# Kernel tuning notes

Hardware: AMD Instinct MI355X
Metric: run time of the kernel (lower is better)

The kernel has to match this reference:

```python
import jax, jax.numpy as jnp
import numpy as np

N_, C_, H_, W_ = 8, 256, 64, 64
HEADS = 8
KS = 3
K2 = KS * KS
OUT = 256
HD = OUT // HEADS
STRIDE = 1
PAD = 1


def setup_inputs() -> dict:
    key = jax.random.key(0)
    ks = jax.random.split(key, 8)
    s = 0.05
    return {
        "input_features": jax.random.normal(ks[0], (N_, C_, H_, W_), jnp.float32),
        "Wq": jax.random.normal(ks[1], (OUT, C_), jnp.float32) * s,
        "Wk": jax.random.normal(ks[2], (OUT, C_), jnp.float32) * s,
        "Wv": jax.random.normal(ks[3], (OUT, C_), jnp.float32) * s,
        "off_w": jax.random.normal(ks[4], (HEADS * K2 * 2, C_, KS, KS), jnp.float32) * 0.01,
        "off_b": jnp.zeros((HEADS * K2 * 2,), jnp.float32),
        "attn_w": jax.random.normal(ks[5], (HEADS * K2, C_, KS, KS), jnp.float32) * 0.01,
        "attn_b": jnp.zeros((HEADS * K2,), jnp.float32),
        "Wo": jax.random.normal(ks[6], (OUT, OUT), jnp.float32) * s,
    }


def _conv2d(x, w, b):
    out = jax.lax.conv_general_dilated(
        x, w, (STRIDE, STRIDE), [(PAD, PAD), (PAD, PAD)],
        dimension_numbers=("NCHW", "OIHW", "NCHW"))
    return out + b[None, :, None, None]


def reference(input_features, Wq, Wk, Wv, off_w, off_b, attn_w, attn_b, Wo):
    x = input_features
    N, C, H, W = x.shape
    # query/key are projected but never used downstream in the original module
    q = jnp.einsum("oc,nchw->nohw", Wq, x)
    k = jnp.einsum("oc,nchw->nohw", Wk, x)
    v = jnp.einsum("oc,nchw->nohw", Wv, x)  # [N, OUT, H, W]

    offsets = _conv2d(x, off_w, off_b)                       # [N, HEADS*K2*2, Ho, Wo]
    aw = jax.nn.sigmoid(_conv2d(x, attn_w, attn_b))          # [N, HEADS*K2, Ho, Wo]
    Ho, Wo_sp = offsets.shape[2], offsets.shape[3]

    gx_base = jnp.linspace(-1.0, 1.0, Wo_sp)
    gy_base = jnp.linspace(-1.0, 1.0, Ho)

    # per-head, per-point (x,y) offsets, scaled by 2/[W,H] as in the source
    off = offsets.reshape(N, HEADS, K2, 2, Ho, Wo_sp)
    gx = gx_base[None, None, None, None, :] + off[:, :, :, 0] * (2.0 / W)  # [N,H,K2,Ho,Wo]
    gy = gy_base[None, None, None, :, None] + off[:, :, :, 1] * (2.0 / H)

    # grid_sample bilinear, align_corners=True, padding_mode='zeros'
    xp = (gx + 1.0) * 0.5 * (W - 1)
    yp = (gy + 1.0) * 0.5 * (H - 1)
    x0 = jnp.floor(xp).astype(jnp.int32)
    y0 = jnp.floor(yp).astype(jnp.int32)
    x1 = x0 + 1
    y1 = y0 + 1
    wx1 = xp - x0
    wx0 = 1.0 - wx1
    wy1 = yp - y0
    wy0 = 1.0 - wy1

    vf = v.reshape(N, HEADS, HD, H * W)

    def corner(yi, xi, wgt):
        valid = ((yi >= 0) & (yi < H) & (xi >= 0) & (xi < W)).astype(v.dtype)
        idx = (jnp.clip(yi, 0, H - 1) * W + jnp.clip(xi, 0, W - 1)).reshape(N, HEADS, -1)
        g = jnp.take_along_axis(vf, idx[:, :, None, :], axis=3)
        g = g.reshape(N, HEADS, HD, K2, Ho, Wo_sp)
        return g * (wgt * valid)[:, :, None]

    sampled = (corner(y0, x0, wy0 * wx0) + corner(y0, x1, wy0 * wx1)
               + corner(y1, x0, wy1 * wx0) + corner(y1, x1, wy1 * wx1))

    awr = aw.reshape(N, HEADS, K2, Ho, Wo_sp)
    head_out = jnp.einsum("nhckxy,nhkxy->nhcxy", sampled, awr)  # weighted sum over K2 points
    combined = head_out.reshape(N, OUT, Ho, Wo_sp)
    return jnp.einsum("oc,nchw->nohw", Wo, combined)
```

## Files before the change

### kernel.cpp

```cpp
#include <hip/hip_runtime.h>
#include <math.h>

#define N_    8
#define C_    256
#define H_    64
#define W_    64
#define HW    4096
#define OUT_  256
#define HEADS 8
#define HD    32
#define K2    9
#define OFFCH 144
#define AWCH  72
#define KTOT  2304
#define WPROWS 256
#define ABASE 16896

typedef __bf16 bf16x8 __attribute__((ext_vector_type(8)));
typedef __bf16 bf16x4 __attribute__((ext_vector_type(4)));
typedef float  f32x4  __attribute__((ext_vector_type(4)));

__device__ __forceinline__ void gload_lds16(const void* g, void* l) {
  __builtin_amdgcn_global_load_lds(
      (const __attribute__((address_space(1))) void*)g,
      (__attribute__((address_space(3))) void*)l, 16, 0, 0);
}

__device__ __forceinline__ void conv_body(
    __bf16* smem, const __bf16* __restrict__ xp, const __bf16* __restrict__ Wp,
    const float* __restrict__ biasp, const __bf16* __restrict__ zbuf,
    __bf16* __restrict__ P2, int yt, int bn, int n, int tid)
{
  const int y0 = yt << 1;
  const int lw = tid & 63, wv = tid >> 6;
  const int lr = lw & 15, lg = lw >> 4;

  f32x4 acc[8][2];
#pragma unroll
  for (int m = 0; m < 8; ++m)
#pragma unroll
    for (int nt = 0; nt < 2; ++nt) acc[m][nt] = (f32x4){0.f, 0.f, 0.f, 0.f};

  if (tid < 64) {
    int p = tid & 3, cs = (tid >> 2) & 1, r = (tid >> 3) & 3, buf = tid >> 5;
    int col = cs ? 65 : 0;
    *(uint4*)&smem[((buf * 4 + r) * 66 + col) * 32 + p * 8] =
        make_uint4(0u, 0u, 0u, 0u);
  }

  int aoff[3][4];
#pragma unroll
  for (int d = 0; d < 3; ++d)
#pragma unroll
    for (int mm = 0; mm < 4; ++mm) {
      int col = (mm << 4) + lr + d;
      int p = lg ^ ((col >> 1) & 3);
      aoff[d][mm] = col * 32 + p * 8;
    }
  int boff[2];
#pragma unroll
  for (int nt = 0; nt < 2; ++nt) {
    int col = (nt << 4) + lr;
    int p = lg ^ ((col >> 1) & 3);
    boff[nt] = ABASE + wv * 3072 + col * 32 + p * 8;
  }

  const int scg = lw & 3;
  const __bf16* gB[2];
#pragma unroll
  for (int jj = 0; jj < 2; ++jj) {
    int col = (jj << 4) + (lw >> 2);
    int cg = scg ^ ((col >> 1) & 3);
    gB[jj] = Wp + (size_t)(bn * 128 + wv * 32 + col) * KTOT + (cg << 3);
  }
  const __bf16* gA[4];
  int aAdd;
  {
    int y = y0 - 1 + wv;
    bool valid = ((unsigned)y < (unsigned)H_);
    aAdd = valid ? 1 : 0;
#pragma unroll
    for (int k = 0; k < 4; ++k) {
      int col = 1 + (k << 4) + (lw >> 2);
      int cg = scg ^ ((col >> 1) & 3);
      gA[k] = valid
          ? xp + ((size_t)(n * HW) + y * W_ + (col - 1)) * C_ + (cg << 3)
          : zbuf;
    }
  }

  auto stageB = [&](int elemOff, int pbuf) {
#pragma unroll
    for (int jj = 0; jj < 2; ++jj)
      gload_lds16(gB[jj] + elemOff,
                  &smem[ABASE + wv * 3072 + pbuf * 1024 + (jj << 9)]);
  };
  auto stageA = [&](int c0elem, int buf) {
    const int add = aAdd ? c0elem : 0;
#pragma unroll
    for (int k = 0; k < 4; ++k)
      gload_lds16(gA[k] + add,
                  &smem[((buf * 4 + wv) * 66 + 1 + (k << 4)) * 32]);
  };

  stageA(0, 0);
  stageB(0 * C_ + 0, 0);
  stageB(1 * C_ + 0, 1);
  asm volatile("s_waitcnt vmcnt(4)" ::: "memory");
  __builtin_amdgcn_s_barrier();
  asm volatile("" ::: "memory");

  for (int cc = 0; cc < 4; ++cc) {
    const bool lastcc = (cc == 3);
#pragma unroll
    for (int sub = 0; sub < 2; ++sub) {
      const int ci = (cc << 1) + sub;
      const int abuf = sub;
#pragma unroll
      for (int tt = 0; tt < 9; ++tt) {
        const int dy = tt / 3, dxp = tt - dy * 3;
        const int pbR = tt % 3;
        const int pbW = (tt + 2) % 3;
        const bool lastSlice = lastcc && (sub == 1);

        if (tt == 1 && ci < 7) stageA((ci + 1) << 5, sub ^ 1);

        if (!(lastSlice && tt >= 7)) {
          const int tn  = (tt < 7) ? (tt + 2) : (tt - 7);
          const int cin = (tt < 7) ? ci : (ci + 1);
          stageB(tn * C_ + (cin << 5), pbW);
        }

        if (lastSlice && tt == 8)
          asm volatile("s_waitcnt vmcnt(0)" ::: "memory");
        else if (lastSlice && tt == 7)
          asm volatile("s_waitcnt vmcnt(2)" ::: "memory");
        else if ((tt == 1 || tt == 2) && ci < 7)
          asm volatile("s_waitcnt vmcnt(8)" ::: "memory");
        else
          asm volatile("s_waitcnt vmcnt(4)" ::: "memory");

        bf16x8 a[8], b[2];
#pragma unroll
        for (int m = 0; m < 8; ++m) {
          const int rr = (m >> 2) + dy;
          a[m] = *(const bf16x8*)&smem[aoff[dxp][m & 3] +
                                       (abuf * 4 + rr) * 2112];
        }
#pragma unroll
        for (int nt = 0; nt < 2; ++nt)
          b[nt] = *(const bf16x8*)&smem[boff[nt] + (pbR << 10)];

        __builtin_amdgcn_s_setprio(1);
#pragma unroll
        for (int m = 0; m < 8; ++m)
#pragma unroll
          for (int nt = 0; nt < 2; ++nt)
            acc[m][nt] = __builtin_amdgcn_mfma_f32_16x16x32_bf16(
                a[m], b[nt], acc[m][nt], 0, 0, 0);
        __builtin_amdgcn_s_setprio(0);

        if (tt == 8 && !lastSlice) {
          __builtin_amdgcn_s_barrier();
          asm volatile("" ::: "memory");
        }
      }
    }
  }

#pragma unroll
  for (int nt = 0; nt < 2; ++nt) {
    const int co = bn * 128 + wv * 32 + (nt << 4) + lr;
    if (co < 216) {
      const float bias = biasp[co];
      int idx;
      if (co < OFFCH) {
        int hh = co / 18;
        idx = (hh << 5) + (co - 18 * hh);
      } else {
        int r = co - OFFCH;
        int hh = r / 9;
        idx = (hh << 5) + 18 + (r - 9 * hh);
      }
#pragma unroll
      for (int m = 0; m < 8; ++m) {
#pragma unroll
        for (int reg = 0; reg < 4; ++reg) {
          const int sl = (m << 4) + (lg << 2) + reg;
          const int yout = y0 + (sl >> 6), xo = sl & 63;
          float v = acc[m][nt][reg] + bias;
          if (co >= OFFCH) v = 1.f / (1.f + expf(-v));
          P2[((size_t)n * HW + yout * W_ + xo) * 256 + idx] = (__bf16)v;
        }
      }
    }
  }
}

template <int MODE>
__device__ __forceinline__ void gemm_body(
    __bf16* smem, const __bf16* __restrict__ A, const __bf16* __restrict__ Wb,
    __bf16* __restrict__ out_b, float* __restrict__ out_f,
    int st, int bn, int n, int tid)
{
  const int s0 = st << 7;
  const int lw = tid & 63, wv = tid >> 6;
  const int lr = lw & 15, lg = lw >> 4;
  const int sm_base = wv << 5;

  f32x4 acc[2][8];
#pragma unroll
  for (int m = 0; m < 2; ++m)
#pragma unroll
    for (int nt = 0; nt < 8; ++nt) acc[m][nt] = (f32x4){0.f, 0.f, 0.f, 0.f};

  int aoff[2];
#pragma unroll
  for (int m = 0; m < 2; ++m) {
    int row = sm_base + (m << 4) + lr;
    int p = lg ^ ((row >> 1) & 3);
    aoff[m] = row * 32 + p * 8;
  }
  int boff[8];
#pragma unroll
  for (int nt = 0; nt < 8; ++nt) {
    int row = (nt << 4) + lr;
    int p = lg ^ ((row >> 1) & 3);
    boff[nt] = 12288 + row * 32 + p * 8;
  }

  const __bf16* gA[2];
  const __bf16* gB[2];
#pragma unroll
  for (int jj = 0; jj < 2; ++jj) {
    int j = wv * 2 + jj;
    int row = (j << 4) + (lw >> 2);
    int cg = (lw & 3) ^ ((row >> 1) & 3);
    gA[jj] = A + ((size_t)n * HW + s0 + row) * 256 + (cg << 3);
    gB[jj] = Wb + ((size_t)((bn << 7) + row)) * 256 + (cg << 3);
  }

  auto stage = [&](int k, int buf) {
    const int koff = k << 5;
#pragma unroll
    for (int jj = 0; jj < 2; ++jj)
      gload_lds16(gA[jj] + koff, &smem[buf * 4096 + ((wv * 2 + jj) << 9)]);
#pragma unroll
    for (int jj = 0; jj < 2; ++jj)
      gload_lds16(gB[jj] + koff,
                  &smem[12288 + buf * 4096 + ((wv * 2 + jj) << 9)]);
  };

  stage(0, 0);
  stage(1, 1);

#pragma unroll
  for (int k = 0; k < 8; ++k) {
    if (k < 7)
      asm volatile("s_waitcnt vmcnt(4)" ::: "memory");
    else
      asm volatile("s_waitcnt vmcnt(0)" ::: "memory");
    __builtin_amdgcn_s_barrier();
    asm volatile("" ::: "memory");

    if (k + 2 < 8) stage(k + 2, (k + 2) % 3);

    const int buf = k % 3;
    bf16x8 a[2], b[8];
#pragma unroll
    for (int m = 0; m < 2; ++m)
      a[m] = *(const bf16x8*)&smem[aoff[m] + buf * 4096];
#pragma unroll
    for (int nt = 0; nt < 8; ++nt)
      b[nt] = *(const bf16x8*)&smem[boff[nt] + buf * 4096];

    __builtin_amdgcn_s_setprio(1);
#pragma unroll
    for (int m = 0; m < 2; ++m)
#pragma unroll
      for (int nt = 0; nt < 8; ++nt)
        acc[m][nt] = __builtin_amdgcn_mfma_f32_16x16x32_bf16(
            a[m], b[nt], acc[m][nt], 0, 0, 0);
    __builtin_amdgcn_s_setprio(0);
  }

#pragma unroll
  for (int m = 0; m < 2; ++m) {
#pragma unroll
    for (int nt = 0; nt < 8; ++nt) {
      const int co = (bn << 7) + (nt << 4) + lr;
      if (MODE == 0) {
#pragma unroll
        for (int reg = 0; reg < 4; ++reg) {
          const int sm = sm_base + (m << 4) + (lg << 2) + reg;
          out_b[((size_t)n * HW + s0 + sm) * 256 + co] = (__bf16)acc[m][nt][reg];
        }
      } else {
        const int sm = sm_base + (m << 4) + (lg << 2);
        float4 v4 = make_float4(acc[m][nt][0], acc[m][nt][1],
                                acc[m][nt][2], acc[m][nt][3]);
        *(float4*)&out_f[((size_t)(n * 256 + co)) * HW + s0 + sm] = v4;
      }
    }
  }
}

__global__ __launch_bounds__(256) void fused_pre_kernel(
    const float* __restrict__ x, __bf16* __restrict__ xp,
    const float* __restrict__ off_w, const float* __restrict__ off_b,
    const float* __restrict__ attn_w, const float* __restrict__ attn_b,
    const float* __restrict__ Wv, const float* __restrict__ Wo,
    __bf16* __restrict__ Wp, float* __restrict__ biasp,
    __bf16* __restrict__ zbuf, __bf16* __restrict__ Wvb,
    __bf16* __restrict__ Wob)
{
  const int b = blockIdx.x;
  const int tid = threadIdx.x;
  __shared__ float tile[64][65];

  if (b < 2048) {
    const int c0 = (b & 3) << 6;
    const int y  = (b >> 2) & 63;
    const int n  = b >> 8;
    const int tx = tid & 63, tg = tid >> 6;
#pragma unroll
    for (int i = 0; i < 16; ++i) {
      int cl = tg + (i << 2);
      tile[cl][tx] = x[((size_t)(n * C_ + c0 + cl) * H_ + y) * W_ + tx];
    }
    __syncthreads();
#pragma unroll
    for (int i = 0; i < 16; ++i) {
      int xl = tg + (i << 2);
      xp[((size_t)(n * HW) + y * W_ + xl) * C_ + c0 + tx] = (__bf16)tile[tx][xl];
    }
  } else {
    const int bb = b - 2048;
    const int c = tid;
    if (bb < 256) {
      const int co = bb;
      if (co == 0) {
        *(uint4*)&zbuf[(size_t)c * 8] = make_uint4(0u, 0u, 0u, 0u);
      }
      const float* base = nullptr;
      if (co < OFFCH)      base = off_w  + ((size_t)co * C_ + c) * 9;
      else if (co < 216)   base = attn_w + ((size_t)(co - OFFCH) * C_ + c) * 9;
#pragma unroll
      for (int t = 0; t < 9; ++t) {
        float w = base ? base[t] : 0.f;
        Wp[(size_t)co * KTOT + t * C_ + c] = (__bf16)w;
      }
      if (c == 0) {
        float bv = 0.f;
        if (co < OFFCH) bv = off_b[co];
        else if (co < 216) bv = attn_b[co - OFFCH];
        biasp[co] = bv;
      }
    } else if (bb < 512) {
      const int i = (bb - 256) * 256 + c;
      Wvb[i] = (__bf16)Wv[i];
    } else {
      const int i = (bb - 512) * 256 + c;
      Wob[i] = (__bf16)Wo[i];
    }
  }
}

__global__ __launch_bounds__(256) void fused_cv_kernel(
    const __bf16* __restrict__ xp, const __bf16* __restrict__ Wp,
    const float* __restrict__ biasp, const __bf16* __restrict__ zbuf,
    __bf16* __restrict__ P2, const __bf16* __restrict__ Wvb,
    __bf16* __restrict__ vtb)
{
  __shared__ __align__(16) __bf16 smem[16896 + 12288];
  const int bn = blockIdx.y;
  if (bn < 2)
    conv_body(smem, xp, Wp, biasp, zbuf, P2, blockIdx.x, bn, blockIdx.z,
              threadIdx.x);
  else
    gemm_body<0>(smem, xp, Wvb, vtb, nullptr, blockIdx.x, bn - 2, blockIdx.z,
                 threadIdx.x);
}

__global__ __launch_bounds__(256) void wo_kernel(
    const __bf16* __restrict__ comb, const __bf16* __restrict__ Wob,
    float* __restrict__ out)
{
  __shared__ __align__(16) __bf16 smem[24576];
  gemm_body<1>(smem, comb, Wob, nullptr, out, blockIdx.x, blockIdx.y,
               blockIdx.z, threadIdx.x);
}

__global__ __launch_bounds__(256) void sample_kernel(
    const __bf16* __restrict__ vtb, const __bf16* __restrict__ P2,
    __bf16* __restrict__ comb)
{
  const int b = blockIdx.x;
  const int y = b & 63;
  const int h = (b >> 6) & 7;
  const int n = b >> 9;
  const int tid = threadIdx.x;
  const int xq = tid >> 2, cg = tid & 3;
  const int lw = tid & 63, wv = tid >> 6;

  __shared__ __align__(16) __bf16 vsl[8 * 64 * 32];

  const int xs = (wv << 4) + (lw >> 2);
  const int cs = lw & 3;
  const __bf16* vrow0 =
      vtb + ((size_t)n * HW) * 256 + (h << 5) + (cs << 3) + (size_t)xs * 256;
#pragma unroll
  for (int r = 0; r < 8; ++r) {
    int yy = y - 3 + r;
    if ((unsigned)yy < (unsigned)H_)
      gload_lds16(vrow0 + (size_t)yy * (64 * 256),
                  &vsl[(r * 64 + (wv << 4)) * 32]);
  }

  const __bf16* prow = P2 + ((size_t)n * HW + y * 64 + xq) * 256 + (h << 5);
  bf16x8 p0 = *(const bf16x8*)(prow);
  bf16x8 p1 = *(const bf16x8*)(prow + 8);
  bf16x8 p2 = *(const bf16x8*)(prow + 16);
  bf16x4 p3 = *(const bf16x4*)(prow + 24);

  __syncthreads();

  float acc[8];
#pragma unroll
  for (int j = 0; j < 8; ++j) acc[j] = 0.f;

  const __bf16* vbase = vtb + ((size_t)n * HW) * 256 + (h << 5) + (cg << 3);

#pragma unroll
  for (int k = 0; k < K2; ++k) {
    float offx, offy, a;
    if (k < 4)      { offx = (float)p0[2 * k];       offy = (float)p0[2 * k + 1]; }
    else if (k < 8) { offx = (float)p1[2 * (k - 4)]; offy = (float)p1[2 * (k - 4) + 1]; }
    else            { offx = (float)p2[0];           offy = (float)p2[1]; }
    if (k < 6)      a = (float)p2[2 + k];
    else            a = (float)p3[k - 6];

    const float xpf = (float)xq + offx * (63.f / 64.f);
    const float ypf = (float)y  + offy * (63.f / 64.f);
    const float fx0 = floorf(xpf), fy0 = floorf(ypf);
    const int x0 = (int)fx0, y0 = (int)fy0;
    const float wx1 = xpf - fx0, wx0 = 1.f - wx1;
    const float wy1 = ypf - fy0, wy0 = 1.f - wy1;

#pragma unroll
    for (int cy = 0; cy < 2; ++cy) {
      const int yi = y0 + cy;
      if ((unsigned)yi >= (unsigned)H_) continue;
      const float wy = cy ? wy1 : wy0;
      const int ridx = yi - (y - 3);
#pragma unroll
      for (int cx = 0; cx < 2; ++cx) {
        const int xi = x0 + cx;
        if ((unsigned)xi >= (unsigned)W_) continue;
        const float cw = a * wy * (cx ? wx1 : wx0);
        bf16x8 v;
        if ((unsigned)ridx < 8u) {
          v = *(const bf16x8*)&vsl[(ridx * 64 + xi) * 32 + (cg << 3)];
        } else {
          v = *(const bf16x8*)(vbase + (size_t)(yi * W_ + xi) * 256);
        }
#pragma unroll
        for (int j = 0; j < 8; ++j) acc[j] = fmaf(cw, (float)v[j], acc[j]);
      }
    }
  }

  bf16x8 r;
#pragma unroll
  for (int j = 0; j < 8; ++j) r[j] = (__bf16)acc[j];
  *(bf16x8*)&comb[((size_t)n * HW + y * 64 + xq) * 256 + (h << 5) + (cg << 3)] = r;
}

extern "C" void kernel_launch(void* const* d_in, const int* in_sizes, int n_in,
                              void* d_out, int out_size, void* d_ws,
                              size_t ws_size, hipStream_t stream)
{
  const float* x      = (const float*)d_in[0];
  const float* Wv     = (const float*)d_in[3];
  const float* off_w  = (const float*)d_in[4];
  const float* off_b  = (const float*)d_in[5];
  const float* attn_w = (const float*)d_in[6];
  const float* attn_b = (const float*)d_in[7];
  const float* Wo     = (const float*)d_in[8];
  float* out = (float*)d_out;

  __bf16* vtb   = (__bf16*)d_ws;
  __bf16* xp    = vtb + (size_t)N_ * HW * OUT_;
  __bf16* comb  = xp + (size_t)N_ * HW * C_;
  __bf16* P2    = comb + (size_t)N_ * HW * OUT_;
  __bf16* Wp    = P2 + (size_t)N_ * HW * 256;
  __bf16* Wvb   = Wp + (size_t)WPROWS * KTOT;
  __bf16* Wob   = Wvb + (size_t)OUT_ * C_;
  __bf16* zbuf  = Wob + (size_t)OUT_ * OUT_;
  float*  biasp = (float*)(zbuf + 2048);

  fused_pre_kernel<<<dim3(2816), 256, 0, stream>>>(
      x, xp, off_w, off_b, attn_w, attn_b, Wv, Wo, Wp, biasp, zbuf, Wvb, Wob);
  fused_cv_kernel<<<dim3(32, 4, N_), 256, 0, stream>>>(xp, Wp, biasp, zbuf, P2,
                                                       Wvb, vtb);
  sample_kernel<<<dim3(N_ * HEADS * H_), 256, 0, stream>>>(vtb, P2, comb);
  wo_kernel<<<dim3(32, 2, N_), 256, 0, stream>>>(comb, Wob, out);
}
```

Measured before the change: 112.9 us.

## Shrink conv tile to one output row per block to double conv block count

The implicit-GEMM conv blocks now compute a single output row (64 pixels) instead of two, so the conv part of the fused grid doubles from 2 to 4 y-slices. The A halo buffer drops from 4 rows to 3 rows, and each wave stages 3 row segments instead of 4, which shrinks shared memory and should raise occupancy and parallelism. In exchange, halo reuse per block falls (3 input rows per output row instead of 4 per 2), and each block re-streams the full weight tile for half the output.

```diff
diff --git a/kernel.cpp b/kernel.cpp
--- a/kernel.cpp
+++ b/kernel.cpp
@@ -14,7 +14,7 @@
 #define AWCH  72
 #define KTOT  2304
 #define WPROWS 256
-#define ABASE 16896
+#define ABASE2 12672
 
 typedef __bf16 bf16x8 __attribute__((ext_vector_type(8)));
 typedef __bf16 bf16x4 __attribute__((ext_vector_type(4)));
@@ -29,22 +29,21 @@
 __device__ __forceinline__ void conv_body(
     __bf16* smem, const __bf16* __restrict__ xp, const __bf16* __restrict__ Wp,
     const float* __restrict__ biasp, const __bf16* __restrict__ zbuf,
-    __bf16* __restrict__ P2, int yt, int bn, int n, int tid)
-{
-  const int y0 = yt << 1;
+    __bf16* __restrict__ P2, int yq, int bn, int n, int tid)
+{
   const int lw = tid & 63, wv = tid >> 6;
   const int lr = lw & 15, lg = lw >> 4;
 
-  f32x4 acc[8][2];
-#pragma unroll
-  for (int m = 0; m < 8; ++m)
+  f32x4 acc[4][2];
+#pragma unroll
+  for (int m = 0; m < 4; ++m)
 #pragma unroll
     for (int nt = 0; nt < 2; ++nt) acc[m][nt] = (f32x4){0.f, 0.f, 0.f, 0.f};
 
-  if (tid < 64) {
-    int p = tid & 3, cs = (tid >> 2) & 1, r = (tid >> 3) & 3, buf = tid >> 5;
+  if (tid < 48) {
+    int p = tid & 3, cs = (tid >> 2) & 1, r = (tid >> 3) % 3, buf = tid / 24;
     int col = cs ? 65 : 0;
-    *(uint4*)&smem[((buf * 4 + r) * 66 + col) * 32 + p * 8] =
+    *(uint4*)&smem[((buf * 3 + r) * 66 + col) * 32 + p * 8] =
         make_uint4(0u, 0u, 0u, 0u);
   }
 
@@ -62,7 +61,7 @@
   for (int nt = 0; nt < 2; ++nt) {
     int col = (nt << 4) + lr;
     int p = lg ^ ((col >> 1) & 3);
-    boff[nt] = ABASE + wv * 3072 + col * 32 + p * 8;
+    boff[nt] = ABASE2 + wv * 3072 + col * 32 + p * 8;
   }
 
   const int scg = lw & 3;
@@ -73,34 +72,35 @@
     int cg = scg ^ ((col >> 1) & 3);
     gB[jj] = Wp + (size_t)(bn * 128 + wv * 32 + col) * KTOT + (cg << 3);
   }
-  const __bf16* gA[4];
-  int aAdd;
-  {
-    int y = y0 - 1 + wv;
+  const __bf16* gA[3];
+  int aAdd[3];
+  int aDst[3];
+#pragma unroll
+  for (int k = 0; k < 3; ++k) {
+    int u = wv * 3 + k;
+    int r = u >> 2, j = u & 3;
+    int y = yq - 1 + r;
     bool valid = ((unsigned)y < (unsigned)H_);
-    aAdd = valid ? 1 : 0;
-#pragma unroll
-    for (int k = 0; k < 4; ++k) {
-      int col = 1 + (k << 4) + (lw >> 2);
-      int cg = scg ^ ((col >> 1) & 3);
-      gA[k] = valid
-          ? xp + ((size_t)(n * HW) + y * W_ + (col - 1)) * C_ + (cg << 3)
-          : zbuf;
-    }
+    aAdd[k] = valid ? 1 : 0;
+    int col = 1 + (j << 4) + (lw >> 2);
+    int cg = scg ^ ((col >> 1) & 3);
+    gA[k] = valid
+        ? xp + ((size_t)(n * HW) + y * W_ + (col - 1)) * C_ + (cg << 3)
+        : zbuf;
+    aDst[k] = (r * 66 + 1 + (j << 4)) * 32;
   }
 
   auto stageB = [&](int elemOff, int pbuf) {
 #pragma unroll
     for (int jj = 0; jj < 2; ++jj)
       gload_lds16(gB[jj] + elemOff,
-                  &smem[ABASE + wv * 3072 + pbuf * 1024 + (jj << 9)]);
+                  &smem[ABASE2 + wv * 3072 + pbuf * 1024 + (jj << 9)]);
   };
   auto stageA = [&](int c0elem, int buf) {
-    const int add = aAdd ? c0elem : 0;
-#pragma unroll
-    for (int k = 0; k < 4; ++k)
-      gload_lds16(gA[k] + add,
-                  &smem[((buf * 4 + wv) * 66 + 1 + (k << 4)) * 32]);
+#pragma unroll
+    for (int k = 0; k < 3; ++k)
+      gload_lds16(gA[k] + (aAdd[k] ? c0elem : 0),
+                  &smem[buf * (3 * 66 * 32) + aDst[k]]);
   };
 
   stageA(0, 0);
@@ -136,24 +136,22 @@
         else if (lastSlice && tt == 7)
           asm volatile("s_waitcnt vmcnt(2)" ::: "memory");
         else if ((tt == 1 || tt == 2) && ci < 7)
-          asm volatile("s_waitcnt vmcnt(8)" ::: "memory");
+          asm volatile("s_waitcnt vmcnt(7)" ::: "memory");
         else
           asm volatile("s_waitcnt vmcnt(4)" ::: "memory");
 
-        bf16x8 a[8], b[2];
-#pragma unroll
-        for (int m = 0; m < 8; ++m) {
-          const int rr = (m >> 2) + dy;
-          a[m] = *(const bf16x8*)&smem[aoff[dxp][m & 3] +
-                                       (abuf * 4 + rr) * 2112];
-        }
+        bf16x8 a[4], b[2];
+#pragma unroll
+        for (int m = 0; m < 4; ++m)
+          a[m] = *(const bf16x8*)&smem[aoff[dxp][m] +
+                                       (abuf * 3 + dy) * 2112];
 #pragma unroll
         for (int nt = 0; nt < 2; ++nt)
           b[nt] = *(const bf16x8*)&smem[boff[nt] + (pbR << 10)];
 
         __builtin_amdgcn_s_setprio(1);
 #pragma unroll
-        for (int m = 0; m < 8; ++m)
+        for (int m = 0; m < 4; ++m)
 #pragma unroll
           for (int nt = 0; nt < 2; ++nt)
             acc[m][nt] = __builtin_amdgcn_mfma_f32_16x16x32_bf16(
@@ -183,14 +181,13 @@
         idx = (hh << 5) + 18 + (r - 9 * hh);
       }
 #pragma unroll
-      for (int m = 0; m < 8; ++m) {
+      for (int m = 0; m < 4; ++m) {
 #pragma unroll
         for (int reg = 0; reg < 4; ++reg) {
-          const int sl = (m << 4) + (lg << 2) + reg;
-          const int yout = y0 + (sl >> 6), xo = sl & 63;
+          const int xo = (m << 4) + (lg << 2) + reg;
           float v = acc[m][nt][reg] + bias;
           if (co >= OFFCH) v = 1.f / (1.f + expf(-v));
-          P2[((size_t)n * HW + yout * W_ + xo) * 256 + idx] = (__bf16)v;
+          P2[((size_t)n * HW + yq * W_ + xo) * 256 + idx] = (__bf16)v;
         }
       }
     }
@@ -372,14 +369,16 @@
     __bf16* __restrict__ P2, const __bf16* __restrict__ Wvb,
     __bf16* __restrict__ vtb)
 {
-  __shared__ __align__(16) __bf16 smem[16896 + 12288];
+  __shared__ __align__(16) __bf16 smem[24960];
   const int bn = blockIdx.y;
-  if (bn < 2)
-    conv_body(smem, xp, Wp, biasp, zbuf, P2, blockIdx.x, bn, blockIdx.z,
-              threadIdx.x);
-  else
-    gemm_body<0>(smem, xp, Wvb, vtb, nullptr, blockIdx.x, bn - 2, blockIdx.z,
+  if (bn < 4) {
+    const int yq  = (blockIdx.x << 1) | (bn & 1);
+    const int cbn = bn >> 1;
+    conv_body(smem, xp, Wp, biasp, zbuf, P2, yq, cbn, blockIdx.z, threadIdx.x);
+  } else {
+    gemm_body<0>(smem, xp, Wvb, vtb, nullptr, blockIdx.x, bn - 4, blockIdx.z,
                  threadIdx.x);
+  }
 }
 
 __global__ __launch_bounds__(256) void wo_kernel(
@@ -501,7 +500,7 @@
 
   fused_pre_kernel<<<dim3(2816), 256, 0, stream>>>(
       x, xp, off_w, off_b, attn_w, attn_b, Wv, Wo, Wp, biasp, zbuf, Wvb, Wob);
-  fused_cv_kernel<<<dim3(32, 4, N_), 256, 0, stream>>>(xp, Wp, biasp, zbuf, P2,
+  fused_cv_kernel<<<dim3(32, 6, N_), 256, 0, stream>>>(xp, Wp, biasp, zbuf, P2,
                                                        Wvb, vtb);
   sample_kernel<<<dim3(N_ * HEADS * H_), 256, 0, stream>>>(vtb, P2, comb);
   wo_kernel<<<dim3(32, 2, N_), 256, 0, stream>>>(comb, Wob, out);
```

Result: slower. 122.8 us (+8.7%).
